# Kernel optimization log

Hardware: AMD Instinct MI355X
Metric: run time of the kernel (lower is better)

The kernel has to match this reference:

```python
import jax, jax.numpy as jnp
import numpy as np

DIM = 1024
NUM_HEADS = 16
HEAD_DIM = DIM // NUM_HEADS
SCALE = 1.0 / DIM ** 0.5  # NOTE: source scales by 1/sqrt(dim), not 1/sqrt(head_dim)


def setup_inputs() -> dict:
    key = jax.random.key(0)
    k1, k2, k3 = jax.random.split(key, 3)
    b, n = 4, 2048
    x = jax.random.normal(k1, (b, n, DIM), dtype=jnp.float32)
    w_qkv = jax.random.normal(k2, (DIM, 3 * DIM), dtype=jnp.float32) * (DIM ** -0.5)
    w_proj = jax.random.normal(k3, (DIM, DIM), dtype=jnp.float32) * (DIM ** -0.5)
    b_proj = jnp.zeros((DIM,), dtype=jnp.float32)
    return {"x": x, "w_qkv": w_qkv, "w_proj": w_proj, "b_proj": b_proj}


def reference(x, w_qkv, w_proj, b_proj):
    b, n, c = x.shape
    h, d = NUM_HEADS, HEAD_DIM
    qkv = (x @ w_qkv).reshape(b, n, 3, h, d)
    qkv = jnp.transpose(qkv, (2, 0, 3, 1, 4))  # [3, b, h, n, d]
    q, k, v = qkv[0], qkv[1], qkv[2]
    attn = jnp.einsum('bhqd,bhkd->bhqk', q, k) * SCALE
    attn = jax.nn.softmax(attn, axis=-1)
    out = jnp.einsum('bhqk,bhkd->bhqd', attn, v)  # [b, h, n, d]
    out = jnp.transpose(out, (0, 2, 1, 3)).reshape(b, n, c)
    return out @ w_proj + b_proj
```

## Files before the change

kernel.cpp:

```cpp
#include <hip/hip_runtime.h>
#include <cstdint>

typedef float f32x4 __attribute__((ext_vector_type(4)));
typedef float f32x16 __attribute__((ext_vector_type(16)));
typedef __bf16 bf16x8 __attribute__((ext_vector_type(8)));
typedef unsigned short u16x4 __attribute__((ext_vector_type(4)));
typedef unsigned short u16x8 __attribute__((ext_vector_type(8)));

__device__ __forceinline__ unsigned short f2bf(float f) {
  union { float f; unsigned u; } x; x.f = f;
  unsigned r = x.u + 0x7FFFu + ((x.u >> 16) & 1u);
  return (unsigned short)(r >> 16);
}

__device__ __forceinline__ void load_lds16(const void* g, void* l) {
  auto gp = reinterpret_cast<const __attribute__((address_space(1))) void*>(
      reinterpret_cast<uintptr_t>(g));
  auto lp = reinterpret_cast<__attribute__((address_space(3))) void*>(
      (unsigned)(reinterpret_cast<uintptr_t>(l)));
  __builtin_amdgcn_global_load_lds(gp, lp, 16, 0, 0);
}


__global__ __launch_bounds__(256) void cvt_x_kernel(const float* __restrict__ in,
                                                    unsigned short* __restrict__ out) {
  const int i = (blockIdx.x * 256 + threadIdx.x) * 8;
  const float4 a = *(const float4*)(in + i);
  const float4 b = *(const float4*)(in + i + 4);
  u16x8 o;
  o[0] = f2bf(a.x); o[1] = f2bf(a.y); o[2] = f2bf(a.z); o[3] = f2bf(a.w);
  o[4] = f2bf(b.x); o[5] = f2bf(b.y); o[6] = f2bf(b.z); o[7] = f2bf(b.w);
  *(u16x8*)(out + i) = o;
}

__global__ __launch_bounds__(256) void cvt_w_t_kernel(const float* __restrict__ W,
                                                      unsigned short* __restrict__ WT,
                                                      int Nw) {
  const int k = blockIdx.y * 256 + threadIdx.x;
  const int n0 = blockIdx.x * 8;
  const float* p = W + (size_t)k * Nw + n0;
  const float4 a = *(const float4*)p;
  const float4 b = *(const float4*)(p + 4);
  float v[8] = {a.x, a.y, a.z, a.w, b.x, b.y, b.z, b.w};
#pragma unroll
  for (int j = 0; j < 8; ++j)
    WT[(size_t)(n0 + j) * 1024 + k] = f2bf(v[j]);
}


template <int EPI>
__global__ __launch_bounds__(256) void gemm_bt(const unsigned short* __restrict__ A,
                                               const unsigned short* __restrict__ BT,
                                               unsigned short* __restrict__ oQ,
                                               unsigned short* __restrict__ oK,
                                               unsigned short* __restrict__ oVT,
                                               float* __restrict__ oF,
                                               const float* __restrict__ bias,
                                               int Ncols) {
  constexpr int K = 1024;
  constexpr int NKT = K / 64;
  __shared__ unsigned short As[2][128 * 64];
  __shared__ unsigned short Bs[2][128 * 64];
  const int tid = threadIdx.x, lane = tid & 63, w = tid >> 6;
  const int wr = w >> 1, wc = w & 1;

  const int nwgx = gridDim.x;
  int id = blockIdx.y * nwgx + blockIdx.x;
  const int cpx = (nwgx * gridDim.y) >> 3;
  id = (id & 7) * cpx + (id >> 3);
  const int mBase = (id / nwgx) * 128, nBase = (id % nwgx) * 128;

  f32x4 acc[4][4];
#pragma unroll
  for (int m = 0; m < 4; ++m)
#pragma unroll
    for (int n = 0; n < 4; ++n)
#pragma unroll
      for (int r = 0; r < 4; ++r) acc[m][n][r] = 0.0f;

  const int srow = lane >> 3;
  const int scol = (lane & 7) * 8;
  const int l15 = lane & 15, g8 = (lane >> 4) * 8;

  auto STAGE = [&](int bufi, int k0_) {
#pragma unroll
    for (int i = 0; i < 4; ++i) {
      const int c = i * 4 + w;
      load_lds16(A + (size_t)(mBase + c * 8 + srow) * K + k0_ + scol, &As[bufi][c * 512]);
      load_lds16(BT + (size_t)(nBase + c * 8 + srow) * K + k0_ + scol, &Bs[bufi][c * 512]);
    }
  };

  STAGE(0, 0);
  __syncthreads();

  for (int kt = 0; kt < NKT; ++kt) {
    const int cur = kt & 1;
    if (kt + 1 < NKT) STAGE(cur ^ 1, (kt + 1) * 64);

    bf16x8 af[4][2], bfr[4][2];
#pragma unroll
    for (int x = 0; x < 4; ++x)
#pragma unroll
      for (int kc = 0; kc < 2; ++kc) {
        af[x][kc] = *(const bf16x8*)&As[cur][(wr * 64 + x * 16 + l15) * 64 + kc * 32 + g8];
        bfr[x][kc] = *(const bf16x8*)&Bs[cur][(wc * 64 + x * 16 + l15) * 64 + kc * 32 + g8];
      }
#pragma unroll
    for (int m = 0; m < 4; ++m)
#pragma unroll
      for (int n = 0; n < 4; ++n)
#pragma unroll
        for (int kc = 0; kc < 2; ++kc)
          acc[m][n] = __builtin_amdgcn_mfma_f32_16x16x32_bf16(af[m][kc], bfr[n][kc],
                                                              acc[m][n], 0, 0, 0);
    __syncthreads();
  }

  const int r0 = (lane >> 4) * 4, c0 = lane & 15;
  if (EPI == 0) {
#pragma unroll
    for (int n = 0; n < 4; ++n) {
      const int col = nBase + wc * 64 + n * 16 + c0;
      const int t = col >> 10, rem = col & 1023;
      const int h = rem >> 6, d = rem & 63;
      if (t == 2) {
#pragma unroll
        for (int m = 0; m < 4; ++m) {
          const int row = mBase + wr * 64 + m * 16 + r0;
          const int b = row >> 11, nn = row & 2047;
          u16x4 o;
#pragma unroll
          for (int r = 0; r < 4; ++r) o[r] = f2bf(acc[m][n][r]);
          *(u16x4*)(oVT + ((size_t)((b * 16 + h) * 64 + d)) * 2048 + nn) = o;
        }
      } else {
        unsigned short* dst = (t == 0) ? oQ : oK;
        const float sc = (t == 0) ? 0.03125f * 1.44269504088896f : 1.0f;
#pragma unroll
        for (int m = 0; m < 4; ++m) {
          const int row = mBase + wr * 64 + m * 16 + r0;
          const int b = row >> 11, nn = row & 2047;
          const size_t base = ((size_t)((b * 16 + h) * 2048 + nn)) * 64 + d;
#pragma unroll
          for (int r = 0; r < 4; ++r)
            dst[base + (size_t)r * 64] = f2bf(acc[m][n][r] * sc);
        }
      }
    }
  } else {
#pragma unroll
    for (int n = 0; n < 4; ++n) {
      const int col = nBase + wc * 64 + n * 16 + c0;
      const float bv = bias[col];
#pragma unroll
      for (int m = 0; m < 4; ++m) {
        const int row = mBase + wr * 64 + m * 16 + r0;
#pragma unroll
        for (int r = 0; r < 4; ++r)
          oF[(size_t)(row + r) * Ncols + col] = acc[m][n][r] + bv;
      }
    }
  }
}


__global__ __launch_bounds__(256) void attn_kernel(const unsigned short* __restrict__ Q,
                                                   const unsigned short* __restrict__ Kt,
                                                   const unsigned short* __restrict__ VT,
                                                   unsigned short* __restrict__ O) {
  __shared__ unsigned short Ks[2][64 * 64];
  __shared__ unsigned short Vs[2][64 * 64];
  __shared__ float Ls[4][32];
  const int tid = threadIdx.x, lane = tid & 63, w = tid >> 6;

  int id = blockIdx.y * gridDim.x + blockIdx.x;
  id = (id & 7) * 128 + (id >> 3);
  const int bh = id >> 4, qt = id & 15;
  const int b = bh >> 4, h = bh & 15;
  const int l31 = lane & 31, hi = lane >> 5;

  const unsigned short* Qp = Q + ((size_t)bh * 2048 + qt * 128 + w * 32) * 64;
  const unsigned short* Kp = Kt + (size_t)bh * 2048 * 64;
  const unsigned short* Vp = VT + (size_t)bh * 64 * 2048;

  bf16x8 qf[4];
#pragma unroll
  for (int ss = 0; ss < 4; ++ss)
    qf[ss] = *(const bf16x8*)(Qp + l31 * 64 + ss * 16 + hi * 8);

  f32x16 accO[2];
#pragma unroll
  for (int db = 0; db < 2; ++db)
#pragma unroll
    for (int r = 0; r < 16; ++r) accO[db][r] = 0.0f;
  float ls = 0.0f;

  const int srow = lane >> 3;
  const int scb = ((lane & 7) * 16) ^ (srow << 4);

  auto STAGE = [&](int bufi, int kt_) {
    const int k0_ = kt_ * 64;
#pragma unroll
    for (int i = 0; i < 2; ++i) {
      const int c = i * 4 + w;
      const int row = c * 8 + srow;
      load_lds16(Kp + (size_t)(k0_ + row) * 64 + (scb >> 1), &Ks[bufi][c * 512]);
      load_lds16(Vp + (size_t)row * 2048 + k0_ + (scb >> 1), &Vs[bufi][c * 512]);
    }
  };

  STAGE(0, 0);
  __syncthreads();

  for (int kt = 0; kt < 32; ++kt) {
    const int cur = kt & 1;
    if (kt + 1 < 32) STAGE(cur ^ 1, kt + 1);

    const char* KsB = (const char*)Ks[cur];
    const char* VsB = (const char*)Vs[cur];

    f32x16 st[2];
#pragma unroll
    for (int kb = 0; kb < 2; ++kb) {
      f32x16 s;
#pragma unroll
      for (int r = 0; r < 16; ++r) s[r] = 0.0f;
      const int row = kb * 32 + l31;
      const int sw = (row & 7) << 4;
#pragma unroll
      for (int ss = 0; ss < 4; ++ss) {
        const bf16x8 kf = *(const bf16x8*)(KsB + row * 128 + ((ss * 32 + hi * 16) ^ sw));
        s = __builtin_amdgcn_mfma_f32_32x32x16_bf16(kf, qf[ss], s, 0, 0, 0);
      }
      st[kb] = s;
    }

    unsigned pk[2][4][2];
#pragma unroll
    for (int kb = 0; kb < 2; ++kb) {
#pragma unroll
      for (int r = 0; r < 16; ++r) {
        const float p = __builtin_amdgcn_exp2f(st[kb][r]);
        st[kb][r] = p;
        ls += p;
      }
#pragma unroll
      for (int m2 = 0; m2 < 4; ++m2)
#pragma unroll
        for (int c = 0; c < 2; ++c)
          asm("v_cvt_pk_bf16_f32 %0, %1, %2"
              : "=v"(pk[kb][m2][c])
              : "v"(st[kb][m2 * 4 + 2 * c]), "v"(st[kb][m2 * 4 + 2 * c + 1]));
    }

    bf16x8 pa[4];
#pragma unroll
    for (int s2 = 0; s2 < 4; ++s2) {
      const int kb = s2 >> 1, t = s2 & 1;
      union { unsigned u[4]; bf16x8 v; } fr;
#pragma unroll
      for (int c = 0; c < 2; ++c) {
        unsigned x = pk[kb][2 * t][c];
        unsigned y = pk[kb][2 * t + 1][c];
        asm("v_permlane32_swap_b32 %0, %1" : "+v"(x), "+v"(y));
        fr.u[c] = x;
        fr.u[2 + c] = y;
      }
      pa[s2] = fr.v;
    }

#pragma unroll
    for (int db = 0; db < 2; ++db) {
      const int row = db * 32 + l31;
      const int sw = (row & 7) << 4;
#pragma unroll
      for (int s2 = 0; s2 < 4; ++s2) {
        const bf16x8 vf = *(const bf16x8*)(VsB + row * 128 + ((s2 * 32 + hi * 16) ^ sw));
        accO[db] = __builtin_amdgcn_mfma_f32_32x32x16_bf16(pa[s2], vf, accO[db], 0, 0, 0);
      }
    }
    __syncthreads();
  }

  ls += __shfl_xor(ls, 32);
  if (hi == 0) Ls[w][l31] = 1.0f / ls;

#pragma unroll
  for (int r = 0; r < 16; ++r) {
    const int ql = (r & 3) + 8 * (r >> 2) + 4 * hi;
    const float inv = Ls[w][ql];
    const size_t base = ((size_t)b * 2048 + qt * 128 + w * 32 + ql) * 1024 + h * 64 + l31;
    O[base] = f2bf(accO[0][r] * inv);
    O[base + 32] = f2bf(accO[1][r] * inv);
  }
}


extern "C" void kernel_launch(void* const* d_in, const int* in_sizes, int n_in,
                              void* d_out, int out_size, void* d_ws, size_t ws_size,
                              hipStream_t stream) {
  const float* x = (const float*)d_in[0];
  const float* w_qkv = (const float*)d_in[1];
  const float* w_proj = (const float*)d_in[2];
  const float* b_proj = (const float*)d_in[3];

  char* ws = (char*)d_ws;
  unsigned short* xb     = (unsigned short*)(ws);
  unsigned short* wqkvT  = (unsigned short*)(ws + 16777216);
  unsigned short* wprojT = (unsigned short*)(ws + 23068672);
  unsigned short* Qb     = (unsigned short*)(ws + 25165824);
  unsigned short* Kb     = (unsigned short*)(ws + 41943040);
  unsigned short* VTb    = (unsigned short*)(ws + 58720256);
  unsigned short* AOb    = (unsigned short*)(ws + 75497472);

  cvt_x_kernel<<<4096, 256, 0, stream>>>(x, xb);
  cvt_w_t_kernel<<<dim3(384, 4), 256, 0, stream>>>(w_qkv, wqkvT, 3072);
  cvt_w_t_kernel<<<dim3(128, 4), 256, 0, stream>>>(w_proj, wprojT, 1024);
  gemm_bt<0><<<dim3(24, 64), 256, 0, stream>>>(xb, wqkvT, Qb, Kb, VTb, nullptr, nullptr, 3072);
  attn_kernel<<<dim3(16, 64), 256, 0, stream>>>(Qb, Kb, VTb, AOb);
  gemm_bt<1><<<dim3(8, 64), 256, 0, stream>>>(AOb, wprojT, nullptr, nullptr, nullptr,
                                              (float*)d_out, b_proj, 1024);
}
```

Measured before the change: 281.0 us.

## Store K in d-chunked layout so attention tiles load and read without swizzle

The QKV GEMM epilogue now writes K as [bh][d/8][n][8] instead of [bh][n][64]. The attention kernel can then stage each 64-key K tile with fully contiguous 16-byte loads per chunk and read fragments with simple linear LDS offsets, without the XOR swizzle. The epilogue's K stores become 2-byte writes with an 8-element stride, which may cost some coalescing on the producer side.

```diff
diff --git a/kernel.cpp b/kernel.cpp
--- a/kernel.cpp
+++ b/kernel.cpp
@@ -124,27 +124,27 @@
       const int col = nBase + wc * 64 + n * 16 + c0;
       const int t = col >> 10, rem = col & 1023;
       const int h = rem >> 6, d = rem & 63;
-      if (t == 2) {
-#pragma unroll
-        for (int m = 0; m < 4; ++m) {
-          const int row = mBase + wr * 64 + m * 16 + r0;
-          const int b = row >> 11, nn = row & 2047;
+#pragma unroll
+      for (int m = 0; m < 4; ++m) {
+        const int row = mBase + wr * 64 + m * 16 + r0;
+        const int b = row >> 11, nn = row & 2047;
+        const int bh = b * 16 + h;
+        if (t == 2) {
           u16x4 o;
 #pragma unroll
           for (int r = 0; r < 4; ++r) o[r] = f2bf(acc[m][n][r]);
-          *(u16x4*)(oVT + ((size_t)((b * 16 + h) * 64 + d)) * 2048 + nn) = o;
-        }
-      } else {
-        unsigned short* dst = (t == 0) ? oQ : oK;
-        const float sc = (t == 0) ? 0.03125f * 1.44269504088896f : 1.0f;
-#pragma unroll
-        for (int m = 0; m < 4; ++m) {
-          const int row = mBase + wr * 64 + m * 16 + r0;
-          const int b = row >> 11, nn = row & 2047;
-          const size_t base = ((size_t)((b * 16 + h) * 2048 + nn)) * 64 + d;
+          *(u16x4*)(oVT + ((size_t)(bh * 64 + d)) * 2048 + nn) = o;
+        } else if (t == 1) {
+          const size_t base = (((size_t)bh * 8 + (d >> 3)) * 2048 + nn) * 8 + (d & 7);
 #pragma unroll
           for (int r = 0; r < 4; ++r)
-            dst[base + (size_t)r * 64] = f2bf(acc[m][n][r] * sc);
+            oK[base + (size_t)r * 8] = f2bf(acc[m][n][r]);
+        } else {
+          const float sc = 0.03125f * 1.44269504088896f;
+          const size_t base = ((size_t)bh * 2048 + nn) * 64 + d;
+#pragma unroll
+          for (int r = 0; r < 4; ++r)
+            oQ[base + (size_t)r * 64] = f2bf(acc[m][n][r] * sc);
         }
       }
     }
@@ -166,10 +166,10 @@
 
 
 __global__ __launch_bounds__(256) void attn_kernel(const unsigned short* __restrict__ Q,
-                                                   const unsigned short* __restrict__ Kt,
+                                                   const unsigned short* __restrict__ Kg,
                                                    const unsigned short* __restrict__ VT,
                                                    unsigned short* __restrict__ O) {
-  __shared__ unsigned short Ks[2][64 * 64];
+  __shared__ unsigned short Ks[2][8 * 512];
   __shared__ unsigned short Vs[2][64 * 64];
   __shared__ float Ls[4][32];
   const int tid = threadIdx.x, lane = tid & 63, w = tid >> 6;
@@ -181,7 +181,7 @@
   const int l31 = lane & 31, hi = lane >> 5;
 
   const unsigned short* Qp = Q + ((size_t)bh * 2048 + qt * 128 + w * 32) * 64;
-  const unsigned short* Kp = Kt + (size_t)bh * 2048 * 64;
+  const unsigned short* Kp = Kg + (size_t)bh * 8 * 2048 * 8;
   const unsigned short* Vp = VT + (size_t)bh * 64 * 2048;
 
   bf16x8 qf[4];
@@ -204,8 +204,8 @@
 #pragma unroll
     for (int i = 0; i < 2; ++i) {
       const int c = i * 4 + w;
+      load_lds16(Kp + ((size_t)c * 2048 + k0_ + lane) * 8, &Ks[bufi][c * 512]);
       const int row = c * 8 + srow;
-      load_lds16(Kp + (size_t)(k0_ + row) * 64 + (scb >> 1), &Ks[bufi][c * 512]);
       load_lds16(Vp + (size_t)row * 2048 + k0_ + (scb >> 1), &Vs[bufi][c * 512]);
     }
   };
@@ -217,7 +217,7 @@
     const int cur = kt & 1;
     if (kt + 1 < 32) STAGE(cur ^ 1, kt + 1);
 
-    const char* KsB = (const char*)Ks[cur];
+    const char* kbase = (const char*)Ks[cur] + hi * 1024 + l31 * 16;
     const char* VsB = (const char*)Vs[cur];
 
     f32x16 st[2];
@@ -226,11 +226,9 @@
       f32x16 s;
 #pragma unroll
       for (int r = 0; r < 16; ++r) s[r] = 0.0f;
-      const int row = kb * 32 + l31;
-      const int sw = (row & 7) << 4;
 #pragma unroll
       for (int ss = 0; ss < 4; ++ss) {
-        const bf16x8 kf = *(const bf16x8*)(KsB + row * 128 + ((ss * 32 + hi * 16) ^ sw));
+        const bf16x8 kf = *(const bf16x8*)(kbase + ss * 2048 + kb * 512);
         s = __builtin_amdgcn_mfma_f32_32x32x16_bf16(kf, qf[ss], s, 0, 0, 0);
       }
       st[kb] = s;
```

After: 282.6 us. Within noise of the previous version (+0.6%).
